# Performance work log

Hardware: AMD Instinct MI355X
Metric: run time of the kernel (lower is better)

The kernel has to match this reference:

```python
import jax, jax.numpy as jnp
import numpy as np

BATCH = 4096
DIM = 512
TEMP = 0.1

def setup_inputs() -> dict:
    key = jax.random.key(0)
    k1, k2 = jax.random.split(key)
    emb_i = jax.random.normal(k1, (BATCH, DIM), dtype=jnp.float32)
    emb_j = jax.random.normal(k2, (BATCH, DIM), dtype=jnp.float32)
    return {"emb_i": emb_i, "emb_j": emb_j}

def _l2_normalize(x, eps=1e-12):
    # matches torch F.normalize(dim=1): x / max(||x||, eps)
    norm = jnp.sqrt(jnp.sum(x * x, axis=1, keepdims=True))
    return x / jnp.maximum(norm, eps)

def reference(emb_i, emb_j):
    n = emb_i.shape[0]
    z_i = _l2_normalize(emb_i)
    z_j = _l2_normalize(emb_j)
    reps = jnp.concatenate([z_i, z_j], axis=0)  # [2N, D], rows unit-norm
    # cosine similarity of unit vectors == dot product -> GEMM instead of O(N^2 D) broadcast
    sim = reps @ reps.T  # [2N, 2N]
    # positives: diag offsets +N and -N
    pos_ij = jnp.sum(z_i * z_j, axis=1)  # diag(sim, +N)
    pos_ji = pos_ij                      # diag(sim, -N) is identical by symmetry
    positives = jnp.concatenate([pos_ij, pos_ji], axis=0)  # [2N]
    nominator = jnp.exp(positives / TEMP)
    neg_mask = 1.0 - jnp.eye(2 * n, dtype=sim.dtype)
    denominator = jnp.sum(neg_mask * jnp.exp(sim / TEMP), axis=1)  # [2N]
    loss_partial = -jnp.log(nominator / denominator)
    return jnp.sum(loss_partial) / (2 * n)
```

## Files before the change

kernel.cpp:

```cpp
#include <hip/hip_runtime.h>
#include <hip/hip_bf16.h>
#include <math.h>

#define N_ROWS 4096
#define DIM    512
#define M_ROWS 8192
#define NTILE  32
#define NB     528
#define NKT    8
#define EXP_SCALE 14.4269504088896340736f

typedef unsigned short ushort_t;
typedef __attribute__((ext_vector_type(8))) short short8;
typedef __attribute__((ext_vector_type(4))) float f32x4;

__device__ __forceinline__ ushort_t f2bf(float x) {
  unsigned int bits = __float_as_uint(x);
  unsigned int lsb = (bits >> 16) & 1u;
  bits += 0x7fffu + lsb;
  return (ushort_t)(bits >> 16);
}

__device__ __forceinline__ void store4bf(ushort_t* p, float4 v, float s) {
  union { ushort_t u[4]; uint2 d; } pk;
  pk.u[0] = f2bf(v.x * s);
  pk.u[1] = f2bf(v.y * s);
  pk.u[2] = f2bf(v.z * s);
  pk.u[3] = f2bf(v.w * s);
  *(uint2*)p = pk.d;
}

__device__ __forceinline__ void async16(const ushort_t* g, ushort_t* l) {
  __builtin_amdgcn_global_load_lds(
      (const __attribute__((address_space(1))) void*)g,
      (__attribute__((address_space(3))) void*)l,
      16, 0, 0);
}

__global__ __launch_bounds__(256) void norm_kernel(
    const float* __restrict__ ei, const float* __restrict__ ej,
    ushort_t* __restrict__ reps, float* __restrict__ pos,
    float* __restrict__ denom) {
  int wave = threadIdx.x >> 6;
  int lane = threadIdx.x & 63;
  int b = blockIdx.x * 4 + wave;
  if (lane == 0) {
    denom[b] = 0.0f;
    denom[b + N_ROWS] = 0.0f;
  }
  const float4* pi = (const float4*)(ei + (size_t)b * DIM);
  const float4* pj = (const float4*)(ej + (size_t)b * DIM);
  float4 a0 = pi[lane];
  float4 a1 = pi[lane + 64];
  float4 b0 = pj[lane];
  float4 b1 = pj[lane + 64];

  float si = a0.x*a0.x + a0.y*a0.y + a0.z*a0.z + a0.w*a0.w
           + a1.x*a1.x + a1.y*a1.y + a1.z*a1.z + a1.w*a1.w;
  float sj = b0.x*b0.x + b0.y*b0.y + b0.z*b0.z + b0.w*b0.w
           + b1.x*b1.x + b1.y*b1.y + b1.z*b1.z + b1.w*b1.w;
  float dp = a0.x*b0.x + a0.y*b0.y + a0.z*b0.z + a0.w*b0.w
           + a1.x*b1.x + a1.y*b1.y + a1.z*b1.z + a1.w*b1.w;

#pragma unroll
  for (int m = 32; m >= 1; m >>= 1) {
    si += __shfl_xor(si, m, 64);
    sj += __shfl_xor(sj, m, 64);
    dp += __shfl_xor(dp, m, 64);
  }
  float ii = 1.0f / fmaxf(sqrtf(si), 1e-12f);
  float ij = 1.0f / fmaxf(sqrtf(sj), 1e-12f);
  if (lane == 0) pos[b] = dp * ii * ij;

  ushort_t* ri = reps + (size_t)b * DIM;
  ushort_t* rj = reps + (size_t)(b + N_ROWS) * DIM;
  store4bf(ri + lane * 4,       a0, ii);
  store4bf(ri + 256 + lane * 4, a1, ii);
  store4bf(rj + lane * 4,       b0, ij);
  store4bf(rj + 256 + lane * 4, b1, ij);
}

__global__ __launch_bounds__(512, 2) void sim_kernel(
    const ushort_t* __restrict__ reps, float* __restrict__ denom) {
  int id = blockIdx.x;
  id = (id & 7) * (NB / 8) + (id >> 3);

  int bi, bj;
  {
    int rem = id, si = 0, sj = 0, found = 0;
    for (int s_j = 0; s_j < 4 && !found; ++s_j)
      for (int s_i = 0; s_i <= s_j && !found; ++s_i) {
        int sz = (s_i == s_j) ? 36 : 64;
        if (rem < sz) { si = s_i; sj = s_j; found = 1; }
        else rem -= sz;
      }
    if (si == sj) {
      int tj = 0;
      while ((tj + 1) * (tj + 2) / 2 <= rem) ++tj;
      int ti = rem - tj * (tj + 1) / 2;
      bi = si * 8 + ti;
      bj = sj * 8 + tj;
    } else {
      bi = si * 8 + (rem & 7);
      bj = sj * 8 + (rem >> 3);
    }
  }
  bool diag = (bi == bj);

  __shared__ ushort_t As[2][2][128 * 64];
  __shared__ ushort_t Bs[2][2][128 * 64];

  int tid  = threadIdx.x;
  int wave = tid >> 6, lane = tid & 63;
  int wr = wave >> 2, wc = wave & 3;
  int hb = wc >> 1;
  int q = lane >> 4, l15 = lane & 15;

  int srow = lane >> 3;
  int scol = ((lane & 7) ^ srow) * 8;
  const ushort_t* pA0 = reps + (size_t)(bi * 256 + wave * 8 + srow) * DIM + scol;
  const ushort_t* pA1 = pA0 + (size_t)128 * DIM;
  const ushort_t* pB0 = reps + (size_t)(bj * 256 + wave * 8 + srow) * DIM + scol;
  const ushort_t* pB1 = pB0 + (size_t)128 * DIM;

#define STAGE_A(D, KOFF) do {                                      \
    ushort_t* la0 = &As[D][0][wave * 512];                         \
    ushort_t* la1 = &As[D][1][wave * 512];                         \
    async16(pA0 + (KOFF),            la0);                         \
    async16(pA0 + 64 * DIM + (KOFF), la0 + 4096);                  \
    async16(pA1 + (KOFF),            la1);                         \
    async16(pA1 + 64 * DIM + (KOFF), la1 + 4096);                  \
  } while (0)

#define STAGE_B(D, KOFF) do {                                      \
    ushort_t* lb0 = &Bs[D][0][wave * 512];                         \
    ushort_t* lb1 = &Bs[D][1][wave * 512];                         \
    async16(pB0 + (KOFF),            lb0);                         \
    async16(pB0 + 64 * DIM + (KOFF), lb0 + 4096);                  \
    async16(pB1 + (KOFF),            lb1);                         \
    async16(pB1 + 64 * DIM + (KOFF), lb1 + 4096);                  \
  } while (0)

  int axor = l15 & 7;
  int aoff0 = l15 * 64 + ((q ^ axor) * 8);
  int aoff1 = l15 * 64 + (((4 + q) ^ axor) * 8);
  int boff0 = (wc & 1) * 4096 + aoff0;
  int boff1 = (wc & 1) * 4096 + aoff1;

  f32x4 zero4 = {0.0f, 0.0f, 0.0f, 0.0f};
  f32x4 acc[8][4];
#pragma unroll
  for (int m = 0; m < 8; ++m)
#pragma unroll
    for (int n = 0; n < 4; ++n) acc[m][n] = zero4;

#define READ_A(DST, MB) do {                                       \
    DST[0][0] = *(const short8*)(Ah + (MB) * 1024 + aoff0);        \
    DST[0][1] = *(const short8*)(Ah + (MB) * 1024 + aoff1);        \
    DST[1][0] = *(const short8*)(Ah + (MB + 1) * 1024 + aoff0);    \
    DST[1][1] = *(const short8*)(Ah + (MB + 1) * 1024 + aoff1);    \
  } while (0)

#define MFMA_PH(MB, AF) do {                                                          \
    _Pragma("unroll")                                                                 \
    for (int n = 0; n < 4; ++n) {                                                     \
      acc[MB][n] = __builtin_amdgcn_mfma_f32_16x16x32_bf16(                           \
          AF[0][0], bfr[0][n], acc[MB][n], 0, 0, 0);                                  \
      acc[MB][n] = __builtin_amdgcn_mfma_f32_16x16x32_bf16(                           \
          AF[0][1], bfr[1][n], acc[MB][n], 0, 0, 0);                                  \
      acc[MB + 1][n] = __builtin_amdgcn_mfma_f32_16x16x32_bf16(                       \
          AF[1][0], bfr[0][n], acc[MB + 1][n], 0, 0, 0);                              \
      acc[MB + 1][n] = __builtin_amdgcn_mfma_f32_16x16x32_bf16(                       \
          AF[1][1], bfr[1][n], acc[MB + 1][n], 0, 0, 0);                              \
    }                                                                                 \
  } while (0)

  STAGE_A(0, 0);
  if (!diag) STAGE_B(0, 0);

  for (int kt = 0; kt < NKT; ++kt) {
    int cur = kt & 1;
    int nk = ((kt + 1) & 7) * 64;
    const ushort_t* Ah = &As[cur][wr][0];
    const ushort_t* Bh = diag ? &As[cur][hb][0] : &Bs[cur][hb][0];

    STAGE_A(cur ^ 1, nk);
    asm volatile("s_waitcnt vmcnt(4)" ::: "memory");
    __builtin_amdgcn_s_barrier();

    short8 bfr[2][4];
#pragma unroll
    for (int n = 0; n < 4; ++n) {
      bfr[0][n] = *(const short8*)(Bh + n * 1024 + boff0);
      bfr[1][n] = *(const short8*)(Bh + n * 1024 + boff1);
    }
    short8 aX[2][2], aY[2][2];
    READ_A(aX, 0);
    READ_A(aY, 2);

    __builtin_amdgcn_s_setprio(1);
    MFMA_PH(0, aX);
    __builtin_amdgcn_s_setprio(0);
    READ_A(aX, 4);
    if (!diag) STAGE_B(cur ^ 1, nk);
    __builtin_amdgcn_s_barrier();

    __builtin_amdgcn_s_setprio(1);
    MFMA_PH(2, aY);
    __builtin_amdgcn_s_setprio(0);
    READ_A(aY, 6);
    __builtin_amdgcn_s_barrier();

    __builtin_amdgcn_s_setprio(1);
    MFMA_PH(4, aX);
    __builtin_amdgcn_s_setprio(0);
    __builtin_amdgcn_s_barrier();

    __builtin_amdgcn_s_setprio(1);
    MFMA_PH(6, aY);
    __builtin_amdgcn_s_setprio(0);
    __builtin_amdgcn_s_barrier();
  }
  asm volatile("s_waitcnt vmcnt(0)" ::: "memory");

  int rowb = bi * 256 + wr * 128 + q * 4;
  int colb = bj * 256 + wc * 64 + l15;

  float rsum[8][4];
  float csum[4] = {0.0f, 0.0f, 0.0f, 0.0f};
#pragma unroll
  for (int m = 0; m < 8; ++m)
#pragma unroll
    for (int r = 0; r < 4; ++r) rsum[m][r] = 0.0f;

#pragma unroll
  for (int m = 0; m < 8; ++m) {
#pragma unroll
    for (int n = 0; n < 4; ++n) {
      f32x4 a = acc[m][n];
#pragma unroll
      for (int r = 0; r < 4; ++r) {
        float v = exp2f(a[r] * EXP_SCALE);
        if (diag && (rowb + m * 16 + r) == (colb + n * 16)) v = 0.0f;
        rsum[m][r] += v;
        csum[n] += v;
      }
    }
  }

#pragma unroll
  for (int m = 0; m < 8; ++m)
#pragma unroll
    for (int r = 0; r < 4; ++r) {
      float v = rsum[m][r];
      v += __shfl_xor(v, 1, 64);
      v += __shfl_xor(v, 2, 64);
      v += __shfl_xor(v, 4, 64);
      v += __shfl_xor(v, 8, 64);
      if (l15 == 0) atomicAdd(&denom[rowb + m * 16 + r], v);
    }

  if (!diag) {
#pragma unroll
    for (int n = 0; n < 4; ++n) {
      float v = csum[n];
      v += __shfl_xor(v, 16, 64);
      v += __shfl_xor(v, 32, 64);
      if (q == 0) atomicAdd(&denom[colb + n * 16], v);
    }
  }
}

__global__ __launch_bounds__(256) void loss_kernel(
    const float* __restrict__ denom, const float* __restrict__ pos,
    float* __restrict__ out) {
  __shared__ float red[4];
  int tid = threadIdx.x;
  float p = 0.0f;
  for (int r = tid; r < M_ROWS; r += 256)
    p += logf(denom[r]) - pos[r & (N_ROWS - 1)] * 10.0f;
#pragma unroll
  for (int m = 32; m >= 1; m >>= 1) p += __shfl_xor(p, m, 64);
  if ((tid & 63) == 0) red[tid >> 6] = p;
  __syncthreads();
  if (tid == 0)
    out[0] = (red[0] + red[1] + red[2] + red[3]) * (1.0f / M_ROWS);
}

extern "C" void kernel_launch(void* const* d_in, const int* in_sizes, int n_in,
                              void* d_out, int out_size, void* d_ws, size_t ws_size,
                              hipStream_t stream) {
  const float* ei = (const float*)d_in[0];
  const float* ej = (const float*)d_in[1];
  float* out = (float*)d_out;

  char* ws = (char*)d_ws;
  ushort_t* reps = (ushort_t*)ws;
  float* denom = (float*)(ws + (size_t)M_ROWS * DIM * 2);
  float* pos = (float*)(ws + (size_t)M_ROWS * DIM * 2 + M_ROWS * 4);

  norm_kernel<<<N_ROWS / 4, 256, 0, stream>>>(ei, ej, reps, pos, denom);
  sim_kernel<<<NB, 512, 0, stream>>>(reps, denom);
  loss_kernel<<<1, 256, 0, stream>>>(denom, pos, out);
}
```

Baseline: 143.9 us.

## Interleave async tile staging across MFMA phases and widen loss reduction block

The next-tile global-to-LDS copies are split into four half-stages, each issued in one of the four MFMA phases, so loads spread across the compute of the current k-tile. Diagonal blocks now also stage B separately instead of reusing the A buffer, which adds redundant loads on those blocks but makes the wait counts uniform. Explicit lgkmcnt waits are placed before each MFMA phase. The final loss kernel now uses 1024 threads instead of 256 to shorten its serial loop.

```diff
diff --git a/kernel.cpp b/kernel.cpp
--- a/kernel.cpp
+++ b/kernel.cpp
@@ -123,22 +123,25 @@
   const ushort_t* pB0 = reps + (size_t)(bj * 256 + wave * 8 + srow) * DIM + scol;
   const ushort_t* pB1 = pB0 + (size_t)128 * DIM;
 
-#define STAGE_A(D, KOFF) do {                                      \
-    ushort_t* la0 = &As[D][0][wave * 512];                         \
-    ushort_t* la1 = &As[D][1][wave * 512];                         \
-    async16(pA0 + (KOFF),            la0);                         \
-    async16(pA0 + 64 * DIM + (KOFF), la0 + 4096);                  \
-    async16(pA1 + (KOFF),            la1);                         \
-    async16(pA1 + 64 * DIM + (KOFF), la1 + 4096);                  \
-  } while (0)
-
-#define STAGE_B(D, KOFF) do {                                      \
-    ushort_t* lb0 = &Bs[D][0][wave * 512];                         \
-    ushort_t* lb1 = &Bs[D][1][wave * 512];                         \
-    async16(pB0 + (KOFF),            lb0);                         \
-    async16(pB0 + 64 * DIM + (KOFF), lb0 + 4096);                  \
-    async16(pB1 + (KOFF),            lb1);                         \
-    async16(pB1 + 64 * DIM + (KOFF), lb1 + 4096);                  \
+#define STAGE2_A0(D, KOFF) do {                                    \
+    ushort_t* l_ = &As[D][0][wave * 512];                          \
+    async16(pA0 + (KOFF),            l_);                          \
+    async16(pA0 + 64 * DIM + (KOFF), l_ + 4096);                   \
+  } while (0)
+#define STAGE2_A1(D, KOFF) do {                                    \
+    ushort_t* l_ = &As[D][1][wave * 512];                          \
+    async16(pA1 + (KOFF),            l_);                          \
+    async16(pA1 + 64 * DIM + (KOFF), l_ + 4096);                   \
+  } while (0)
+#define STAGE2_B0(D, KOFF) do {                                    \
+    ushort_t* l_ = &Bs[D][0][wave * 512];                          \
+    async16(pB0 + (KOFF),            l_);                          \
+    async16(pB0 + 64 * DIM + (KOFF), l_ + 4096);                   \
+  } while (0)
+#define STAGE2_B1(D, KOFF) do {                                    \
+    ushort_t* l_ = &Bs[D][1][wave * 512];                          \
+    async16(pB1 + (KOFF),            l_);                          \
+    async16(pB1 + 64 * DIM + (KOFF), l_ + 4096);                   \
   } while (0)
 
   int axor = l15 & 7;
@@ -175,18 +178,20 @@
     }                                                                                 \
   } while (0)
 
-  STAGE_A(0, 0);
-  if (!diag) STAGE_B(0, 0);
+  STAGE2_A0(0, 0);
+  STAGE2_A1(0, 0);
+  STAGE2_B0(0, 0);
+  STAGE2_B1(0, 0);
 
   for (int kt = 0; kt < NKT; ++kt) {
-    int cur = kt & 1;
+    int cur = kt & 1, nxt = cur ^ 1;
     int nk = ((kt + 1) & 7) * 64;
     const ushort_t* Ah = &As[cur][wr][0];
-    const ushort_t* Bh = diag ? &As[cur][hb][0] : &Bs[cur][hb][0];
-
-    STAGE_A(cur ^ 1, nk);
-    asm volatile("s_waitcnt vmcnt(4)" ::: "memory");
-    __builtin_amdgcn_s_barrier();
+    const ushort_t* Bh = &Bs[cur][hb][0];
+
+    STAGE2_A0(nxt, nk);
+    asm volatile("s_waitcnt vmcnt(2)" ::: "memory");
+    asm volatile("s_barrier" ::: "memory");
 
     short8 bfr[2][4];
 #pragma unroll
@@ -194,30 +199,35 @@
       bfr[0][n] = *(const short8*)(Bh + n * 1024 + boff0);
       bfr[1][n] = *(const short8*)(Bh + n * 1024 + boff1);
     }
-    short8 aX[2][2], aY[2][2];
-    READ_A(aX, 0);
-    READ_A(aY, 2);
-
+    short8 aE[2][2], aO[2][2];
+    READ_A(aE, 0);
+    asm volatile("s_waitcnt lgkmcnt(0)" ::: "memory");
     __builtin_amdgcn_s_setprio(1);
-    MFMA_PH(0, aX);
-    __builtin_amdgcn_s_setprio(0);
-    READ_A(aX, 4);
-    if (!diag) STAGE_B(cur ^ 1, nk);
-    __builtin_amdgcn_s_barrier();
-
-    __builtin_amdgcn_s_setprio(1);
-    MFMA_PH(2, aY);
-    __builtin_amdgcn_s_setprio(0);
-    READ_A(aY, 6);
-    __builtin_amdgcn_s_barrier();
-
-    __builtin_amdgcn_s_setprio(1);
-    MFMA_PH(4, aX);
+    MFMA_PH(0, aE);
     __builtin_amdgcn_s_setprio(0);
     __builtin_amdgcn_s_barrier();
 
+    STAGE2_A1(nxt, nk);
+    READ_A(aO, 2);
+    asm volatile("s_waitcnt lgkmcnt(0)" ::: "memory");
     __builtin_amdgcn_s_setprio(1);
-    MFMA_PH(6, aY);
+    MFMA_PH(2, aO);
+    __builtin_amdgcn_s_setprio(0);
+    __builtin_amdgcn_s_barrier();
+
+    STAGE2_B0(nxt, nk);
+    READ_A(aE, 4);
+    asm volatile("s_waitcnt lgkmcnt(0)" ::: "memory");
+    __builtin_amdgcn_s_setprio(1);
+    MFMA_PH(4, aE);
+    __builtin_amdgcn_s_setprio(0);
+    __builtin_amdgcn_s_barrier();
+
+    STAGE2_B1(nxt, nk);
+    READ_A(aO, 6);
+    asm volatile("s_waitcnt lgkmcnt(0)" ::: "memory");
+    __builtin_amdgcn_s_setprio(1);
+    MFMA_PH(6, aO);
     __builtin_amdgcn_s_setprio(0);
     __builtin_amdgcn_s_barrier();
   }
@@ -271,20 +281,24 @@
   }
 }
 
-__global__ __launch_bounds__(256) void loss_kernel(
+__global__ __launch_bounds__(1024) void loss_kernel(
     const float* __restrict__ denom, const float* __restrict__ pos,
     float* __restrict__ out) {
-  __shared__ float red[4];
+  __shared__ float red[16];
   int tid = threadIdx.x;
   float p = 0.0f;
-  for (int r = tid; r < M_ROWS; r += 256)
+  for (int r = tid; r < M_ROWS; r += 1024)
     p += logf(denom[r]) - pos[r & (N_ROWS - 1)] * 10.0f;
 #pragma unroll
   for (int m = 32; m >= 1; m >>= 1) p += __shfl_xor(p, m, 64);
   if ((tid & 63) == 0) red[tid >> 6] = p;
   __syncthreads();
-  if (tid == 0)
-    out[0] = (red[0] + red[1] + red[2] + red[3]) * (1.0f / M_ROWS);
+  if (tid == 0) {
+    float s = 0.0f;
+#pragma unroll
+    for (int i = 0; i < 16; ++i) s += red[i];
+    out[0] = s * (1.0f / M_ROWS);
+  }
 }
 
 extern "C" void kernel_launch(void* const* d_in, const int* in_sizes, int n_in,
@@ -301,5 +315,5 @@
 
   norm_kernel<<<N_ROWS / 4, 256, 0, stream>>>(ei, ej, reps, pos, denom);
   sim_kernel<<<NB, 512, 0, stream>>>(reps, denom);
-  loss_kernel<<<1, 256, 0, stream>>>(denom, pos, out);
-}
+  loss_kernel<<<1, 1024, 0, stream>>>(denom, pos, out);
+}
```

Result: no change. 143.9 us (+0.0%).
